# Performance work log

Hardware: AMD Instinct MI355X
Metric: run time of the kernel (lower is better)

The kernel has to match this reference:

```python
import jax, jax.numpy as jnp
import numpy as np

D_MODEL = 256
N_HEADS = 4
WINDOW = 8
DECAY = 0.9
STEP_SIZE = 0.5


def _linear(x, w, b):
    # torch nn.Linear: y = x @ w.T + b, w: [out, in]
    return jnp.einsum('...i,oi->...o', x, w) + b


def _layernorm(x, scale, bias, eps=1e-5):
    mu = jnp.mean(x, axis=-1, keepdims=True)
    var = jnp.var(x, axis=-1, keepdims=True)
    return (x - mu) * jax.lax.rsqrt(var + eps) * scale + bias


def _ema(x, decay):
    # ema[t] = decay*ema[t-1] + (1-decay)*x[t], ema[-1]=0
    # (exactly the causal conv with weights (1-d)*d^i from the torch code)
    def step(c, xt):
        c = decay * c + (1.0 - decay) * xt
        return c, c
    _, ys = jax.lax.scan(step, jnp.zeros_like(x[:, 0]), jnp.swapaxes(x, 0, 1))
    return jnp.swapaxes(ys, 0, 1)


def setup_inputs() -> dict:
    key = jax.random.key(0)
    ks = iter(jax.random.split(key, 40))
    B, T, D = 8, 1024, D_MODEL
    s = 0.02
    inp = {
        'parallel_repr': jax.random.normal(next(ks), (B, T, D), jnp.float32),
        'sequential_state': jax.random.normal(next(ks), (B, D), jnp.float32),
        'trajectory_summary': jax.random.normal(next(ks), (B, D), jnp.float32),
        # MultiheadAttention params
        'in_proj_w': jax.random.normal(next(ks), (3 * D, D), jnp.float32) * s,
        'in_proj_b': jnp.zeros((3 * D,), jnp.float32),
        'out_proj_w': jax.random.normal(next(ks), (D, D), jnp.float32) * s,
        'out_proj_b': jnp.zeros((D,), jnp.float32),
        # depthwise causal conv (local history)
        'conv_w': jax.random.normal(next(ks), (D, 1, WINDOW), jnp.float32) * s,
        'conv_b': jnp.zeros((D,), jnp.float32),
        # parallel_to_sequential / sequential_to_parallel
        'p2s_w': jax.random.normal(next(ks), (D, D), jnp.float32) * s,
        'p2s_b': jnp.zeros((D,), jnp.float32),
        's2p_w': jax.random.normal(next(ks), (D, D), jnp.float32) * s,
        's2p_b': jnp.zeros((D,), jnp.float32),
        # transition MLP: 3D -> 2D -> D
        'trans_w1': jax.random.normal(next(ks), (2 * D, 3 * D), jnp.float32) * s,
        'trans_b1': jnp.zeros((2 * D,), jnp.float32),
        'trans_w2': jax.random.normal(next(ks), (D, 2 * D), jnp.float32) * s,
        'trans_b2': jnp.zeros((D,), jnp.float32),
        # FFN: D -> 4D -> D
        'ffn_w1': jax.random.normal(next(ks), (4 * D, D), jnp.float32) * s,
        'ffn_b1': jnp.zeros((4 * D,), jnp.float32),
        'ffn_w2': jax.random.normal(next(ks), (D, 4 * D), jnp.float32) * s,
        'ffn_b2': jnp.zeros((D,), jnp.float32),
        # LayerNorms
        'ln1_s': jnp.ones((D,), jnp.float32), 'ln1_b': jnp.zeros((D,), jnp.float32),
        'ln2_s': jnp.ones((D,), jnp.float32), 'ln2_b': jnp.zeros((D,), jnp.float32),
        'ln3_s': jnp.ones((D,), jnp.float32), 'ln3_b': jnp.zeros((D,), jnp.float32),
        'ln4_s': jnp.ones((D,), jnp.float32), 'ln4_b': jnp.zeros((D,), jnp.float32),
    }
    return inp


def _forward(parallel_repr, sequential_state,
             in_proj_w, in_proj_b, out_proj_w, out_proj_b,
             conv_w, conv_b, p2s_w, p2s_b, s2p_w, s2p_b,
             trans_w1, trans_b1, trans_w2, trans_b2,
             ffn_w1, ffn_b1, ffn_w2, ffn_b2,
             ln1_s, ln1_b, ln2_s, ln2_b, ln3_s, ln3_b, ln4_s, ln4_b):
    B, T, D = parallel_repr.shape
    H, hd = N_HEADS, D // N_HEADS

    # --- causal self-attention (nn.MultiheadAttention, batch_first) ---
    qkv = _linear(parallel_repr, in_proj_w, in_proj_b)
    q, k, v = jnp.split(qkv, 3, axis=-1)
    q = q.reshape(B, T, H, hd)
    k = k.reshape(B, T, H, hd)
    v = v.reshape(B, T, H, hd)
    scores = jnp.einsum('bqhd,bkhd->bhqk', q, k) / jnp.sqrt(jnp.asarray(hd, q.dtype))
    causal = jnp.triu(jnp.ones((T, T), bool), 1)
    scores = jnp.where(causal, jnp.finfo(scores.dtype).min, scores)
    attn = jax.nn.softmax(scores, axis=-1)
    attn_out = jnp.einsum('bhqk,bkhd->bqhd', attn, v).reshape(B, T, D)
    attn_out = _linear(attn_out, out_proj_w, out_proj_b)
    x = _layernorm(parallel_repr + attn_out, ln1_s, ln1_b)

    # --- depthwise causal conv (local history) ---
    xt = jnp.swapaxes(x, 1, 2)  # [B, D, T]
    xt_pad = jnp.pad(xt, ((0, 0), (0, 0), (WINDOW - 1, 0)))
    local = jax.lax.conv_general_dilated(
        xt_pad, conv_w, window_strides=(1,), padding='VALID',
        dimension_numbers=('NCH', 'OIH', 'NCH'), feature_group_count=D)
    local_history = jnp.swapaxes(local + conv_b[None, :, None], 1, 2)  # [B, T, D]

    # --- global EMA summary ---
    global_summary = _ema(x, DECAY)

    # --- transition deltas + cumsum state integration ---
    parallel_guidance = _linear(x, p2s_w, p2s_b)
    combined = jnp.concatenate([x + 0.3 * parallel_guidance, local_history, global_summary], axis=-1)
    h = jax.nn.gelu(_linear(combined, trans_w1, trans_b1), approximate=False)
    deltas = _linear(h, trans_w2, trans_b2)
    states = sequential_state[:, None, :] + jnp.cumsum(deltas, axis=1) * STEP_SIZE
    states = _layernorm(states, ln3_s, ln3_b)

    # --- FFN with sequential guidance ---
    seq_guidance = _linear(states, s2p_w, s2p_b)
    f = jax.nn.gelu(_linear(x + 0.3 * seq_guidance, ffn_w1, ffn_b1), approximate=False)
    ffn_out = _linear(f, ffn_w2, ffn_b2)
    x = _layernorm(x + ffn_out, ln2_s, ln2_b)

    final_sequential_state = _layernorm(states[:, -1, :], ln4_s, ln4_b)
    final_trajectory_summary = global_summary[:, -1, :]
    return x, final_sequential_state, final_trajectory_summary


def reference(parallel_repr, sequential_state, trajectory_summary,
              in_proj_w, in_proj_b, out_proj_w, out_proj_b,
              conv_w, conv_b, p2s_w, p2s_b, s2p_w, s2p_b,
              trans_w1, trans_b1, trans_w2, trans_b2,
              ffn_w1, ffn_b1, ffn_w2, ffn_b2,
              ln1_s, ln1_b, ln2_s, ln2_b, ln3_s, ln3_b, ln4_s, ln4_b):
    # trajectory_summary is accepted by the torch forward but never used.
    return _forward(parallel_repr, sequential_state,
                    in_proj_w, in_proj_b, out_proj_w, out_proj_b,
                    conv_w, conv_b, p2s_w, p2s_b, s2p_w, s2p_b,
                    trans_w1, trans_b1, trans_w2, trans_b2,
                    ffn_w1, ffn_b1, ffn_w2, ffn_b2,
                    ln1_s, ln1_b, ln2_s, ln2_b, ln3_s, ln3_b, ln4_s, ln4_b)
```

## Files before the change

kernel.cpp:

```cpp
#include <hip/hip_runtime.h>
#include <math.h>

typedef unsigned short u16;
typedef __attribute__((ext_vector_type(8))) short bf16x8;
typedef __attribute__((ext_vector_type(4))) float f32x4;

#define D_MODEL 256
#define T_SZ 1024
constexpr size_t S_ELT = (size_t)8192 * 256;
constexpr size_t MB = 1024 * 1024;

constexpr size_t OFF_QKV = 0;
constexpr size_t OFF_ATTN = 12 * MB;
constexpr size_t OFF_F = 0;
constexpr size_t OFF_X = 16 * MB;
constexpr size_t OFF_COMB = 24 * MB;
constexpr size_t OFF_FB = 36 * MB;
constexpr size_t OFF_H = 44 * MB;
constexpr size_t OFF_WB = 52 * MB;
constexpr int WB_INPROJ = 0;
constexpr int WB_OUTPROJ = 196608;
constexpr int WB_P2S = 262144;
constexpr int WB_S2P = 327680;
constexpr int WB_T1 = 393216;
constexpr int WB_T2 = 786432;
constexpr int WB_F1 = 917504;
constexpr int WB_F2 = 1179648;
constexpr int WB_TOTAL = 1441792;
constexpr int PR_TOTAL = 2097152;
constexpr size_t OFF_B1E = OFF_WB + (size_t)WB_TOTAL * 2;
constexpr size_t OFF_B1E2 = OFF_B1E + 4096;
constexpr size_t OFF_WC2 = 55 * MB;
constexpr size_t OFF_SCR1 = 55 * MB + 524288;
constexpr size_t OFF_SCR2 = 55 * MB + 786432;

__device__ __forceinline__ u16 f2bf(float f) {
  unsigned int u = __float_as_uint(f);
  u += 0x7fff + ((u >> 16) & 1);
  return (u16)(u >> 16);
}
__device__ __forceinline__ float bf2f(u16 s) {
  return __uint_as_float(((unsigned int)s) << 16);
}

__device__ __forceinline__ void glds16(const u16* g, u16* l) {
  __builtin_amdgcn_global_load_lds(
      (const __attribute__((address_space(1))) void*)g,
      (__attribute__((address_space(3))) void*)l, 16, 0, 0);
}

__global__ __launch_bounds__(256)
void wconv_kernel(const float* w0, const float* w1, const float* w2,
                  const float* w3, const float* w4, const float* w5,
                  const float* w6, const float* w7, const float* pr,
                  u16* __restrict__ wb, u16* __restrict__ prb) {
  const int idx4 = (blockIdx.x * 256 + threadIdx.x) * 4;
  if (idx4 < WB_TOTAL) {
    const int offs[9] = {WB_INPROJ, WB_OUTPROJ, WB_P2S,  WB_S2P, WB_T1,
                         WB_T2,     WB_F1,      WB_F2,   WB_TOTAL};
    const float* srcs[8] = {w0, w1, w2, w3, w4, w5, w6, w7};
    int seg = 0;
    while (idx4 >= offs[seg + 1]) ++seg;
    float4 v = *(const float4*)(srcs[seg] + (idx4 - offs[seg]));
    unsigned int lo = (unsigned int)f2bf(v.x) | ((unsigned int)f2bf(v.y) << 16);
    unsigned int hi = (unsigned int)f2bf(v.z) | ((unsigned int)f2bf(v.w) << 16);
    *(uint2*)(wb + idx4) = make_uint2(lo, hi);
  } else {
    const int i4 = idx4 - WB_TOTAL;
    if (i4 < PR_TOTAL) {
      float4 v = *(const float4*)(pr + i4);
      unsigned int lo = (unsigned int)f2bf(v.x) | ((unsigned int)f2bf(v.y) << 16);
      unsigned int hi = (unsigned int)f2bf(v.z) | ((unsigned int)f2bf(v.w) << 16);
      *(uint2*)(prb + i4) = make_uint2(lo, hi);
    }
  }
}

__global__ __launch_bounds__(256)
void wfold_kernel(const float* __restrict__ t1, const float* __restrict__ p2s,
                  const float* __restrict__ t1b, const float* __restrict__ p2sb,
                  const float* __restrict__ f1, const float* __restrict__ s2p,
                  const float* __restrict__ f1b, const float* __restrict__ s2pb,
                  u16* __restrict__ wt1, float* __restrict__ b1e,
                  u16* __restrict__ wc2, float* __restrict__ b1e2) {
  __shared__ float trow[8][256];
  const int blk = blockIdx.x;
  const int k = threadIdx.x;
  const bool t1role = blk < 64;
  const int o0 = t1role ? blk * 8 : (blk - 64) * 8;
  const float* wsrc = t1role ? t1 : f1;
  const int wstride = t1role ? 768 : 256;
  const float* psrc = t1role ? p2s : s2p;
  const float* pbsrc = t1role ? p2sb : s2pb;
#pragma unroll
  for (int r = 0; r < 8; ++r)
    trow[r][k] = wsrc[(size_t)(o0 + r) * wstride + k];
  __syncthreads();
  float acc[8] = {};
  float bacc[8] = {};
  for (int i = 0; i < 256; ++i) {
    const float pv = psrc[(size_t)i * 256 + k];
    const float pbv = pbsrc[i];
#pragma unroll
    for (int r = 0; r < 8; ++r) {
      acc[r] = fmaf(trow[r][i], pv, acc[r]);
      bacc[r] = fmaf(trow[r][i], pbv, bacc[r]);
    }
  }
  if (t1role) {
#pragma unroll
    for (int r = 0; r < 8; ++r)
      wt1[(size_t)(o0 + r) * 768 + k] = f2bf(trow[r][k] + 0.3f * acc[r]);
    if (k == 0) {
#pragma unroll
      for (int r = 0; r < 8; ++r)
        b1e[o0 + r] = t1b[o0 + r] + 0.3f * bacc[r];
    }
  } else {
#pragma unroll
    for (int r = 0; r < 8; ++r)
      wc2[(size_t)(o0 + r) * 256 + k] = f2bf(0.3f * acc[r]);
    if (k == 0) {
#pragma unroll
      for (int r = 0; r < 8; ++r)
        b1e2[o0 + r] = f1b[o0 + r] + 0.3f * bacc[r];
    }
  }
}

enum { EPI_NONE = 0, EPI_GELU = 1 };

template <int EPI, int BM, int BN, bool OUTBF, bool VSPLIT, bool SPLIT>
__global__ __launch_bounds__(256, 4)
void mgemm(const u16* __restrict__ A, int lda, const u16* __restrict__ A2,
           const u16* __restrict__ Wb, int ldb, const u16* __restrict__ B2,
           int K, const float* __restrict__ bias, void* __restrict__ Cv,
           int ldc, int col_off, u16* __restrict__ vt) {
  __shared__ u16 As[2 * BM * 64];
  __shared__ u16 Bs[2 * BN * 64];
  const int tid = threadIdx.x;
  const int w = tid >> 6, lane = tid & 63;
  const int ln = lane & 15, quad = lane >> 4;
  const int m0 = blockIdx.x * BM;
  const int n0 = blockIdx.y * BN;
  constexpr int MT = (BM == 128) ? 2 : 1;
  const int wm = w * (MT * 16);
  constexpr int APW = BM / 64;
  constexpr int BPW = BN / 64;

  f32x4 acc[MT][4] = {};

  const int grow = lane >> 2;
  const int gk8 = (lane & 3) * 8;

#define STAGE_MM(k0s, buf)                                                    \
  {                                                                           \
    const u16* Ag; const u16* Bg; int as_, bs_, kk;                           \
    if (!SPLIT || (k0s) < 256) {                                              \
      Ag = A; as_ = lda; Bg = Wb; bs_ = ldb; kk = (k0s);                      \
    } else {                                                                  \
      Ag = A2; as_ = 256; Bg = B2; bs_ = 256; kk = (k0s)-256;                 \
    }                                                                         \
    _Pragma("unroll") for (int s = 0; s < 2; ++s) {                           \
      _Pragma("unroll") for (int p = 0; p < APW; ++p) {                       \
        const int g = w * APW + p;                                            \
        glds16(Ag + (size_t)(m0 + g * 16 + grow) * as_ + kk + s * 32 + gk8,   \
               As + (buf) * (BM * 64) + s * BM * 32 + g * 512);               \
      }                                                                       \
      _Pragma("unroll") for (int p = 0; p < BPW; ++p) {                       \
        const int g = w * BPW + p;                                            \
        glds16(Bg + (size_t)(n0 + g * 16 + grow) * bs_ + kk + s * 32 + gk8,   \
               Bs + (buf) * (BN * 64) + s * BN * 32 + g * 512);               \
      }                                                                       \
    }                                                                         \
  }

  int cur = 0;
  STAGE_MM(0, 0);
  for (int k0 = 0; k0 < K; k0 += 64) {
    __syncthreads();
    if (k0 + 64 < K) STAGE_MM(k0 + 64, cur ^ 1);
#pragma unroll
    for (int s = 0; s < 2; ++s) {
      const u16* abase =
          As + cur * (BM * 64) + s * BM * 32 + (wm >> 4) * 512 + ln * 32 + quad * 8;
      const u16* bbase = Bs + cur * (BN * 64) + s * BN * 32 + ln * 32 + quad * 8;
      bf16x8 af[MT], bv[4];
#pragma unroll
      for (int i = 0; i < MT; ++i) af[i] = *(const bf16x8*)(abase + i * 512);
#pragma unroll
      for (int j = 0; j < 4; ++j) bv[j] = *(const bf16x8*)(bbase + j * 512);
#pragma unroll
      for (int i = 0; i < MT; ++i)
#pragma unroll
        for (int j = 0; j < 4; ++j)
          acc[i][j] = __builtin_amdgcn_mfma_f32_16x16x32_bf16(af[i], bv[j],
                                                              acc[i][j], 0, 0, 0);
    }
    cur ^= 1;
  }
#undef STAGE_MM

#pragma unroll
  for (int i = 0; i < MT; ++i)
#pragma unroll
    for (int j = 0; j < 4; ++j) {
      const int col = n0 + j * 16 + ln;
      const float bsv = bias[col];
      const int row0 = m0 + wm + i * 16 + quad * 4;
      float vals[4];
#pragma unroll
      for (int r = 0; r < 4; ++r) {
        float v = acc[i][j][r] + bsv;
        if (EPI == EPI_GELU) v = 0.5f * v * (1.0f + erff(v * 0.70710678f));
        vals[r] = v;
      }
      if (VSPLIT && col >= 512) {
        ushort4 pk;
        pk.x = f2bf(vals[0]); pk.y = f2bf(vals[1]);
        pk.z = f2bf(vals[2]); pk.w = f2bf(vals[3]);
        *(ushort4*)(vt + (size_t)((row0 >> 10) * 256 + (col - 512)) * T_SZ +
                    (row0 & 1023)) = pk;
      } else if (OUTBF) {
#pragma unroll
        for (int r = 0; r < 4; ++r)
          ((u16*)Cv)[(size_t)(row0 + r) * ldc + col_off + col] = f2bf(vals[r]);
      } else {
#pragma unroll
        for (int r = 0; r < 4; ++r)
          ((float*)Cv)[(size_t)(row0 + r) * ldc + col_off + col] = vals[r];
      }
    }
}

template <bool WRITE_BF>
__global__ __launch_bounds__(256, 4)
void mgemm_ln16(const u16* __restrict__ A, const u16* __restrict__ Wb, int K,
                const float* __restrict__ bias, const float* __restrict__ addsrc,
                const float* __restrict__ g, const float* __restrict__ bb,
                float* __restrict__ outf, u16* __restrict__ outbf, int bfldc) {
  __shared__ u16 As[2 * 1024];
  __shared__ u16 Bs[2 * 16384];
  __shared__ float tS1[4][16], tS2[4][16];
  const int tid = threadIdx.x;
  const int w = tid >> 6, lane = tid & 63;
  const int ln = lane & 15, quad = lane >> 4;
  const int m0 = blockIdx.x * 16;
  const int grow = lane >> 2;
  const int gk8 = (lane & 3) * 8;

  f32x4 acc[4] = {};

#define STAGE_LN(k0s, buf)                                                    \
  {                                                                           \
    if (w < 2)                                                                \
      glds16(A + (size_t)(m0 + grow) * K + (k0s) + w * 32 + gk8,              \
             As + (buf) * 1024 + w * 512);                                    \
    _Pragma("unroll") for (int p = 0; p < 8; ++p) {                           \
      const int idx = w * 8 + p;                                              \
      const int s = idx >> 4, gg = idx & 15;                                  \
      glds16(Wb + (size_t)(gg * 16 + grow) * K + (k0s) + s * 32 + gk8,        \
             Bs + (buf) * 16384 + s * 8192 + gg * 512);                       \
    }                                                                         \
  }

  int cur = 0;
  STAGE_LN(0, 0);
  for (int k0 = 0; k0 < K; k0 += 64) {
    __syncthreads();
    if (k0 + 64 < K) STAGE_LN(k0 + 64, cur ^ 1);
#pragma unroll
    for (int s = 0; s < 2; ++s) {
      const bf16x8 af =
          *(const bf16x8*)(As + cur * 1024 + s * 512 + ln * 32 + quad * 8);
      const u16* bbase =
          Bs + cur * 16384 + s * 8192 + (w * 4) * 512 + ln * 32 + quad * 8;
#pragma unroll
      for (int j = 0; j < 4; ++j) {
        bf16x8 bv = *(const bf16x8*)(bbase + j * 512);
        acc[j] = __builtin_amdgcn_mfma_f32_16x16x32_bf16(af, bv, acc[j], 0, 0, 0);
      }
    }
    cur ^= 1;
  }
#undef STAGE_LN

  const int row0 = m0 + quad * 4;
  float s1[4] = {}, s2[4] = {};
#pragma unroll
  for (int j = 0; j < 4; ++j) {
    const int col = w * 64 + j * 16 + ln;
    const float bsv = bias[col];
#pragma unroll
    for (int r = 0; r < 4; ++r) {
      float v = acc[j][r] + bsv + addsrc[(size_t)(row0 + r) * 256 + col];
      acc[j][r] = v;
      s1[r] += v;
      s2[r] += v * v;
    }
  }
#pragma unroll
  for (int r = 0; r < 4; ++r) {
#pragma unroll
    for (int o = 8; o > 0; o >>= 1) {
      s1[r] += __shfl_xor(s1[r], o);
      s2[r] += __shfl_xor(s2[r], o);
    }
  }
  __syncthreads();
  if (ln == 0) {
#pragma unroll
    for (int r = 0; r < 4; ++r) {
      tS1[w][quad * 4 + r] = s1[r];
      tS2[w][quad * 4 + r] = s2[r];
    }
  }
  __syncthreads();
  float mean[4], inv[4];
#pragma unroll
  for (int r = 0; r < 4; ++r) {
    const int qr = quad * 4 + r;
    const float S1 = tS1[0][qr] + tS1[1][qr] + tS1[2][qr] + tS1[3][qr];
    const float S2 = tS2[0][qr] + tS2[1][qr] + tS2[2][qr] + tS2[3][qr];
    mean[r] = S1 * (1.f / 256.f);
    const float var = S2 * (1.f / 256.f) - mean[r] * mean[r];
    inv[r] = rsqrtf(var + 1e-5f);
  }
#pragma unroll
  for (int j = 0; j < 4; ++j) {
    const int col = w * 64 + j * 16 + ln;
    const float gc = g[col], bc = bb[col];
#pragma unroll
    for (int r = 0; r < 4; ++r) {
      const float y = (acc[j][r] - mean[r]) * inv[r] * gc + bc;
      outf[(size_t)(row0 + r) * 256 + col] = y;
      if (WRITE_BF) outbf[(size_t)(row0 + r) * bfldc + col] = f2bf(y);
    }
  }
}

__global__ __launch_bounds__(256)
void attn_flash(const u16* __restrict__ qkv, const u16* __restrict__ vt,
                u16* __restrict__ outp) {
  __shared__ u16 Ks[2][4096];
  __shared__ u16 Vs[2][4096];
  __shared__ u16 Ps[4][16][72];
  const int tid = threadIdx.x;
  const int w = tid >> 6, lane = tid & 63;
  const int ln = lane & 15, quad = lane >> 4, kq8 = quad * 8;
  const int bid = blockIdx.x;
  const int r0 = bid & 255;
  int bh = r0 >> 4;
  int p = r0 & 15;
  if (bid >> 8) { bh += 16; p = 15 - p; }
  const int qt = p * 4 + w;
  const int q0 = qt * 16;
  const int b = bh >> 2, h = bh & 3;
  const u16* base = qkv + (size_t)b * T_SZ * 768;
  const u16* kbase = base + 256 + h * 64;
  const u16* vbase = vt + (size_t)bh * 64 * T_SZ;
  const int grow = lane >> 2;
  const int gk8 = (lane & 3) * 8;

  bf16x8 qf[2];
#pragma unroll
  for (int ks = 0; ks < 2; ++ks)
    qf[ks] = *(const bf16x8*)(base + (size_t)(q0 + ln) * 768 + h * 64 +
                              ks * 32 + kq8);
  const short ob = (short)0x3F80;
  const bf16x8 ones = {ob, ob, ob, ob, ob, ob, ob, ob};

  const int nt = p + 1;

#define STAGE_KV(jt, buf)                                                     \
  {                                                                           \
    const int c0s = (jt) * 64;                                                \
    const int isV = w >> 1, ss = w & 1;                                       \
    _Pragma("unroll") for (int pg = 0; pg < 4; ++pg) {                        \
      if (!isV)                                                               \
        glds16(kbase + (size_t)(c0s + pg * 16 + grow) * 768 + ss * 32 + gk8,  \
               &Ks[buf][ss * 2048 + pg * 512]);                               \
      else                                                                    \
        glds16(vbase + (size_t)(pg * 16 + grow) * T_SZ + c0s + ss * 32 + gk8, \
               &Vs[buf][ss * 2048 + pg * 512]);                               \
    }                                                                         \
  }

  f32x4 O[4] = {};
  f32x4 l_acc = {};
  int cur = 0;
  STAGE_KV(0, 0);
  for (int jt = 0; jt < nt; ++jt) {
    __syncthreads();
    if (jt + 1 < nt) STAGE_KV(jt + 1, cur ^ 1);
    const int c0 = jt * 64;
    f32x4 sv[4] = {};
#pragma unroll
    for (int ks = 0; ks < 2; ++ks)
#pragma unroll
      for (int j = 0; j < 4; ++j) {
        bf16x8 kf = *(const bf16x8*)&Ks[cur][ks * 2048 + j * 512 + ln * 32 + kq8];
        sv[j] = __builtin_amdgcn_mfma_f32_16x16x32_bf16(qf[ks], kf, sv[j], 0, 0, 0);
      }
    const bool need_mask = (jt == nt - 1);
#pragma unroll
    for (int j = 0; j < 4; ++j)
#pragma unroll
      for (int r = 0; r < 4; ++r) {
        float pv = __expf(sv[j][r] * 0.125f);
        if (need_mask && (c0 + j * 16 + ln > q0 + quad * 4 + r)) pv = 0.f;
        Ps[w][quad * 4 + r][j * 16 + ln] = f2bf(pv);
      }
#pragma unroll
    for (int ks = 0; ks < 2; ++ks) {
      bf16x8 pf = *(const bf16x8*)&Ps[w][ln][ks * 32 + kq8];
      l_acc = __builtin_amdgcn_mfma_f32_16x16x32_bf16(pf, ones, l_acc, 0, 0, 0);
#pragma unroll
      for (int j = 0; j < 4; ++j) {
        bf16x8 vf = *(const bf16x8*)&Vs[cur][ks * 2048 + j * 512 + ln * 32 + kq8];
        O[j] = __builtin_amdgcn_mfma_f32_16x16x32_bf16(pf, vf, O[j], 0, 0, 0);
      }
    }
    cur ^= 1;
  }
#undef STAGE_KV

  u16* op = outp + (size_t)b * T_SZ * 256;
#pragma unroll
  for (int r = 0; r < 4; ++r) {
    const float inv = 1.f / l_acc[r];
#pragma unroll
    for (int j = 0; j < 4; ++j)
      op[(size_t)(q0 + quad * 4 + r) * 256 + h * 64 + j * 16 + ln] =
          f2bf(O[j][r] * inv);
  }
}

__device__ __forceinline__ void block_reduce_2(float& a, float& q, float* tmp) {
#pragma unroll
  for (int o = 32; o > 0; o >>= 1) {
    a += __shfl_down(a, o);
    q += __shfl_down(q, o);
  }
  const int lane = threadIdx.x & 63, wid = threadIdx.x >> 6;
  if (lane == 0) { tmp[wid] = a; tmp[4 + wid] = q; }
  __syncthreads();
  a = tmp[0] + tmp[1] + tmp[2] + tmp[3];
  q = tmp[4] + tmp[5] + tmp[6] + tmp[7];
  __syncthreads();
}

__device__ __forceinline__ float ln_finish(float v, float s1, float s2,
                                           float g, float bb) {
  float mean = s1 * (1.f / 256.f);
  float var = s2 * (1.f / 256.f) - mean * mean;
  return (v - mean) * rsqrtf(var + 1e-5f) * g + bb;
}

__global__ __launch_bounds__(256)
void emaconv_kernel(const float* __restrict__ x, const float* __restrict__ cw,
                    const float* __restrict__ cb, u16* __restrict__ comb,
                    float* __restrict__ scr) {
  const int bc = blockIdx.x;
  const int b = bc >> 5, ch = bc & 31;
  const int d = threadIdx.x;
  const int t0 = ch * 32;
  float wreg[8];
#pragma unroll
  for (int j = 0; j < 8; ++j) wreg[j] = cw[d * 8 + j];
  const float bias = cb[d];
  float xw[8];
#pragma unroll
  for (int j = 0; j < 7; ++j) {
    const int ts = t0 - 7 + j;
    xw[j] = (ts >= 0) ? x[(size_t)(b * T_SZ + ts) * 256 + d] : 0.f;
  }
  float c = 0.f;
#pragma unroll
  for (int tl = 0; tl < 32; ++tl) {
    const size_t row = (size_t)(b * T_SZ + t0 + tl);
    xw[7] = x[row * 256 + d];
    float conv = bias;
#pragma unroll
    for (int j = 0; j < 8; ++j) conv = fmaf(xw[j], wreg[j], conv);
    c = 0.9f * c + 0.1f * xw[7];
    comb[row * 768 + 256 + d] = f2bf(conv);
    comb[row * 768 + 512 + d] = f2bf(c);
#pragma unroll
    for (int j = 0; j < 7; ++j) xw[j] = xw[j + 1];
  }
  scr[(size_t)bc * 256 + d] = c;
}

__global__ __launch_bounds__(256)
void ema_b_kernel(float* __restrict__ scr) {
  const int b = blockIdx.x, d = threadIdx.x;
  const float q32 = 0.03433683820292512f;
  float carry = 0.f;
  for (int ch = 0; ch < 32; ++ch) {
    const size_t idx = (size_t)(b * 32 + ch) * 256 + d;
    float e = scr[idx];
    scr[idx] = carry;
    carry = e + q32 * carry;
  }
}

__global__ __launch_bounds__(256)
void ema_c_kernel(u16* __restrict__ comb, const float* __restrict__ scr,
                  float* __restrict__ fts) {
  const int row = blockIdx.x;
  const int b = row >> 10, t = row & 1023;
  const int d = threadIdx.x;
  const int ch = t >> 5, tl = t & 31;
  float carry = scr[(size_t)(b * 32 + ch) * 256 + d];
  float l = bf2f(comb[(size_t)row * 768 + 512 + d]);
  float y = fmaf(__powf(0.9f, (float)(tl + 1)), carry, l);
  comb[(size_t)row * 768 + 512 + d] = f2bf(y);
  if (t == 1023) fts[b * 256 + d] = y;
}

__global__ __launch_bounds__(256)
void cs_a_kernel(float* __restrict__ deltas, float* __restrict__ scr) {
  const int bc = blockIdx.x;
  const int b = bc >> 5, ch = bc & 31;
  const int d = threadIdx.x;
  const int t0 = ch * 32;
  float c = 0.f;
  for (int tl = 0; tl < 32; ++tl) {
    const size_t idx = (size_t)(b * T_SZ + t0 + tl) * 256 + d;
    c += deltas[idx];
    deltas[idx] = c;
  }
  scr[(size_t)bc * 256 + d] = c;
}

__global__ __launch_bounds__(256)
void cs_b_kernel(float* __restrict__ scr) {
  const int b = blockIdx.x, d = threadIdx.x;
  float carry = 0.f;
  for (int ch = 0; ch < 32; ++ch) {
    const size_t idx = (size_t)(b * 32 + ch) * 256 + d;
    float e = scr[idx];
    scr[idx] = carry;
    carry += e;
  }
}

__global__ __launch_bounds__(256)
void ln3_states_kernel(const float* __restrict__ deltas, const float* __restrict__ scr,
                       const float* __restrict__ seq, const float* __restrict__ g3,
                       const float* __restrict__ b3, const float* __restrict__ g4,
                       const float* __restrict__ b4, u16* __restrict__ st,
                       float* __restrict__ fss) {
  __shared__ float tmp[8];
  const int row = blockIdx.x;
  const int b = row >> 10, t = row & 1023;
  const int d = threadIdx.x;
  float v = seq[b * 256 + d] +
            0.5f * (deltas[(size_t)row * 256 + d] +
                    scr[(size_t)(b * 32 + (t >> 5)) * 256 + d]);
  float a = v, q = v * v;
  block_reduce_2(a, q, tmp);
  const float y = ln_finish(v, a, q, g3[d], b3[d]);
  st[(size_t)row * 256 + d] = f2bf(y);
  if (t == 1023) {
    float a2 = y, q2 = y * y;
    block_reduce_2(a2, q2, tmp);
    fss[b * 256 + d] = ln_finish(y, a2, q2, g4[d], b4[d]);
  }
}

extern "C" void kernel_launch(void* const* d_in, const int* in_sizes, int n_in,
                              void* d_out, int out_size, void* d_ws,
                              size_t ws_size, hipStream_t stream) {
  (void)in_sizes; (void)n_in; (void)out_size; (void)ws_size;
  const float* parallel_repr = (const float*)d_in[0];
  const float* sequential_state = (const float*)d_in[1];
  const float* in_proj_b = (const float*)d_in[4];
  const float* out_proj_b = (const float*)d_in[6];
  const float* conv_w = (const float*)d_in[7];
  const float* conv_b = (const float*)d_in[8];
  const float* p2s_w_f = (const float*)d_in[9];
  const float* p2s_b = (const float*)d_in[10];
  const float* s2p_w_f = (const float*)d_in[11];
  const float* s2p_b = (const float*)d_in[12];
  const float* trans_w1_f = (const float*)d_in[13];
  const float* trans_b1 = (const float*)d_in[14];
  const float* trans_b2 = (const float*)d_in[16];
  const float* ffn_w1_f = (const float*)d_in[17];
  const float* ffn_b1 = (const float*)d_in[18];
  const float* ffn_b2 = (const float*)d_in[20];
  const float* ln1_s = (const float*)d_in[21];
  const float* ln1_b = (const float*)d_in[22];
  const float* ln2_s = (const float*)d_in[23];
  const float* ln2_b = (const float*)d_in[24];
  const float* ln3_s = (const float*)d_in[25];
  const float* ln3_b = (const float*)d_in[26];
  const float* ln4_s = (const float*)d_in[27];
  const float* ln4_b = (const float*)d_in[28];

  char* ws = (char*)d_ws;
  u16* qkv_bf = (u16*)(ws + OFF_QKV);
  u16* attn_bf = (u16*)(ws + OFF_ATTN);
  u16* states_bf = (u16*)(ws + OFF_ATTN);
  u16* f_bf = (u16*)(ws + OFF_F);
  float* x = (float*)(ws + OFF_X);
  u16* comb = (u16*)(ws + OFF_COMB);
  u16* pr_bf = (u16*)(ws + OFF_COMB);
  float* fbuf = (float*)(ws + OFF_FB);
  u16* vt = (u16*)(ws + OFF_H);
  u16* h_bf = (u16*)(ws + OFF_H);
  u16* wb = (u16*)(ws + OFF_WB);
  u16* wc2 = (u16*)(ws + OFF_WC2);
  float* scr1 = (float*)(ws + OFF_SCR1);
  float* scr2 = (float*)(ws + OFF_SCR2);
  float* b1e = (float*)(ws + OFF_B1E);
  float* b1e2 = (float*)(ws + OFF_B1E2);
  float* out = (float*)d_out;
  float* out_fss = out + S_ELT;
  float* out_fts = out + S_ELT + 2048;

  const dim3 blk(256);

  wconv_kernel<<<3456, blk, 0, stream>>>(
      (const float*)d_in[3], (const float*)d_in[5], (const float*)d_in[9],
      (const float*)d_in[11], (const float*)d_in[13], (const float*)d_in[15],
      (const float*)d_in[17], (const float*)d_in[19], parallel_repr, wb, pr_bf);
  wfold_kernel<<<192, blk, 0, stream>>>(trans_w1_f, p2s_w_f, trans_b1, p2s_b,
                                        ffn_w1_f, s2p_w_f, ffn_b1, s2p_b,
                                        wb + WB_T1, b1e, wc2, b1e2);
  mgemm<EPI_NONE, 128, 64, true, true, false><<<dim3(64, 12), blk, 0, stream>>>(
      pr_bf, 256, nullptr, wb + WB_INPROJ, 256, nullptr, 256, in_proj_b,
      qkv_bf, 768, 0, vt);
  attn_flash<<<512, blk, 0, stream>>>(qkv_bf, vt, attn_bf);
  mgemm_ln16<true><<<512, blk, 0, stream>>>(
      attn_bf, wb + WB_OUTPROJ, 256, out_proj_b, parallel_repr, ln1_s, ln1_b,
      x, comb, 768);
  emaconv_kernel<<<256, blk, 0, stream>>>(x, conv_w, conv_b, comb, scr1);
  ema_b_kernel<<<8, blk, 0, stream>>>(scr1);
  ema_c_kernel<<<8192, blk, 0, stream>>>(comb, scr1, out_fts);
  mgemm<EPI_GELU, 128, 64, true, false, false><<<dim3(64, 8), blk, 0, stream>>>(
      comb, 768, nullptr, wb + WB_T1, 768, nullptr, 768, b1e, h_bf, 512, 0,
      nullptr);
  mgemm<EPI_NONE, 64, 64, false, false, false><<<dim3(128, 4), blk, 0, stream>>>(
      h_bf, 512, nullptr, wb + WB_T2, 512, nullptr, 512, trans_b2, fbuf, 256,
      0, nullptr);
  cs_a_kernel<<<256, blk, 0, stream>>>(fbuf, scr2);
  cs_b_kernel<<<8, blk, 0, stream>>>(scr2);
  ln3_states_kernel<<<8192, blk, 0, stream>>>(fbuf, scr2, sequential_state,
                                              ln3_s, ln3_b, ln4_s, ln4_b,
                                              states_bf, out_fss);
  mgemm<EPI_GELU, 128, 64, true, false, true><<<dim3(64, 16), blk, 0, stream>>>(
      comb, 768, states_bf, wb + WB_F1, 256, wc2, 512, b1e2, f_bf, 1024, 0,
      nullptr);
  mgemm_ln16<false><<<512, blk, 0, stream>>>(
      f_bf, wb + WB_F2, 1024, ffn_b2, x, ln2_s, ln2_b, out, nullptr, 256);
}
```

Baseline: 263.3 us.

## Merge weight prep kernels, fuse chunked cumsum into GEMM epilogue, vectorize EMA fixup

After: 269.7 us. +2.4%, slower.

```diff
diff --git a/kernel.cpp b/kernel.cpp
--- a/kernel.cpp
+++ b/kernel.cpp
@@ -50,92 +50,96 @@
 }
 
 __global__ __launch_bounds__(256)
-void wconv_kernel(const float* w0, const float* w1, const float* w2,
+void wprep_kernel(const float* w0, const float* w1, const float* w2,
                   const float* w3, const float* w4, const float* w5,
                   const float* w6, const float* w7, const float* pr,
-                  u16* __restrict__ wb, u16* __restrict__ prb) {
-  const int idx4 = (blockIdx.x * 256 + threadIdx.x) * 4;
-  if (idx4 < WB_TOTAL) {
-    const int offs[9] = {WB_INPROJ, WB_OUTPROJ, WB_P2S,  WB_S2P, WB_T1,
-                         WB_T2,     WB_F1,      WB_F2,   WB_TOTAL};
-    const float* srcs[8] = {w0, w1, w2, w3, w4, w5, w6, w7};
-    int seg = 0;
-    while (idx4 >= offs[seg + 1]) ++seg;
-    float4 v = *(const float4*)(srcs[seg] + (idx4 - offs[seg]));
-    unsigned int lo = (unsigned int)f2bf(v.x) | ((unsigned int)f2bf(v.y) << 16);
-    unsigned int hi = (unsigned int)f2bf(v.z) | ((unsigned int)f2bf(v.w) << 16);
-    *(uint2*)(wb + idx4) = make_uint2(lo, hi);
+                  u16* __restrict__ wb, u16* __restrict__ prb,
+                  const float* __restrict__ t1b, const float* __restrict__ p2sb,
+                  const float* __restrict__ f1b, const float* __restrict__ s2pb,
+                  float* __restrict__ b1e, u16* __restrict__ wc2,
+                  float* __restrict__ b1e2) {
+  __shared__ float trow[8][256];
+  const int bx = blockIdx.x;
+  if (bx < 3456) {
+    const int idx4 = (bx * 256 + threadIdx.x) * 4;
+    if (idx4 < WB_TOTAL) {
+      const int offs[9] = {WB_INPROJ, WB_OUTPROJ, WB_P2S,  WB_S2P, WB_T1,
+                           WB_T2,     WB_F1,      WB_F2,   WB_TOTAL};
+      const float* srcs[8] = {w0, w1, w2, w3, w4, w5, w6, w7};
+      int seg = 0;
+      while (idx4 >= offs[seg + 1]) ++seg;
+      const bool skip = (seg == 4) && (((idx4 - WB_T1) % 768) < 256);
+      if (!skip) {
+        float4 v = *(const float4*)(srcs[seg] + (idx4 - offs[seg]));
+        unsigned int lo = (unsigned int)f2bf(v.x) | ((unsigned int)f2bf(v.y) << 16);
+        unsigned int hi = (unsigned int)f2bf(v.z) | ((unsigned int)f2bf(v.w) << 16);
+        *(uint2*)(wb + idx4) = make_uint2(lo, hi);
+      }
+    } else {
+      const int i4 = idx4 - WB_TOTAL;
+      if (i4 < PR_TOTAL) {
+        float4 v = *(const float4*)(pr + i4);
+        unsigned int lo = (unsigned int)f2bf(v.x) | ((unsigned int)f2bf(v.y) << 16);
+        unsigned int hi = (unsigned int)f2bf(v.z) | ((unsigned int)f2bf(v.w) << 16);
+        *(uint2*)(prb + i4) = make_uint2(lo, hi);
+      }
+    }
   } else {
-    const int i4 = idx4 - WB_TOTAL;
-    if (i4 < PR_TOTAL) {
-      float4 v = *(const float4*)(pr + i4);
-      unsigned int lo = (unsigned int)f2bf(v.x) | ((unsigned int)f2bf(v.y) << 16);
-      unsigned int hi = (unsigned int)f2bf(v.z) | ((unsigned int)f2bf(v.w) << 16);
-      *(uint2*)(prb + i4) = make_uint2(lo, hi);
-    }
-  }
-}
-
-__global__ __launch_bounds__(256)
-void wfold_kernel(const float* __restrict__ t1, const float* __restrict__ p2s,
-                  const float* __restrict__ t1b, const float* __restrict__ p2sb,
-                  const float* __restrict__ f1, const float* __restrict__ s2p,
-                  const float* __restrict__ f1b, const float* __restrict__ s2pb,
-                  u16* __restrict__ wt1, float* __restrict__ b1e,
-                  u16* __restrict__ wc2, float* __restrict__ b1e2) {
-  __shared__ float trow[8][256];
-  const int blk = blockIdx.x;
-  const int k = threadIdx.x;
-  const bool t1role = blk < 64;
-  const int o0 = t1role ? blk * 8 : (blk - 64) * 8;
-  const float* wsrc = t1role ? t1 : f1;
-  const int wstride = t1role ? 768 : 256;
-  const float* psrc = t1role ? p2s : s2p;
-  const float* pbsrc = t1role ? p2sb : s2pb;
-#pragma unroll
-  for (int r = 0; r < 8; ++r)
-    trow[r][k] = wsrc[(size_t)(o0 + r) * wstride + k];
-  __syncthreads();
-  float acc[8] = {};
-  float bacc[8] = {};
-  for (int i = 0; i < 256; ++i) {
-    const float pv = psrc[(size_t)i * 256 + k];
-    const float pbv = pbsrc[i];
-#pragma unroll
-    for (int r = 0; r < 8; ++r) {
-      acc[r] = fmaf(trow[r][i], pv, acc[r]);
-      bacc[r] = fmaf(trow[r][i], pbv, bacc[r]);
-    }
-  }
-  if (t1role) {
+    const int blk = bx - 3456;
+    const int k = threadIdx.x;
+    const bool t1role = blk < 64;
+    const int o0 = t1role ? blk * 8 : (blk - 64) * 8;
+    const float* wsrc = t1role ? w4 : w6;
+    const int wstride = t1role ? 768 : 256;
+    const float* psrc = t1role ? w2 : w3;
+    const float* pbsrc = t1role ? p2sb : s2pb;
 #pragma unroll
     for (int r = 0; r < 8; ++r)
-      wt1[(size_t)(o0 + r) * 768 + k] = f2bf(trow[r][k] + 0.3f * acc[r]);
-    if (k == 0) {
+      trow[r][k] = wsrc[(size_t)(o0 + r) * wstride + k];
+    __syncthreads();
+    float acc[8] = {};
+    float bacc[8] = {};
+    for (int i = 0; i < 256; ++i) {
+      const float pv = psrc[(size_t)i * 256 + k];
+      const float pbv = pbsrc[i];
+#pragma unroll
+      for (int r = 0; r < 8; ++r) {
+        acc[r] = fmaf(trow[r][i], pv, acc[r]);
+        bacc[r] = fmaf(trow[r][i], pbv, bacc[r]);
+      }
+    }
+    if (t1role) {
+      u16* wt1 = wb + WB_T1;
 #pragma unroll
       for (int r = 0; r < 8; ++r)
-        b1e[o0 + r] = t1b[o0 + r] + 0.3f * bacc[r];
-    }
-  } else {
-#pragma unroll
-    for (int r = 0; r < 8; ++r)
-      wc2[(size_t)(o0 + r) * 256 + k] = f2bf(0.3f * acc[r]);
-    if (k == 0) {
+        wt1[(size_t)(o0 + r) * 768 + k] = f2bf(trow[r][k] + 0.3f * acc[r]);
+      if (k == 0) {
+#pragma unroll
+        for (int r = 0; r < 8; ++r)
+          b1e[o0 + r] = t1b[o0 + r] + 0.3f * bacc[r];
+      }
+    } else {
 #pragma unroll
       for (int r = 0; r < 8; ++r)
-        b1e2[o0 + r] = f1b[o0 + r] + 0.3f * bacc[r];
+        wc2[(size_t)(o0 + r) * 256 + k] = f2bf(0.3f * acc[r]);
+      if (k == 0) {
+#pragma unroll
+        for (int r = 0; r < 8; ++r)
+          b1e2[o0 + r] = f1b[o0 + r] + 0.3f * bacc[r];
+      }
     }
   }
 }
 
 enum { EPI_NONE = 0, EPI_GELU = 1 };
 
-template <int EPI, int BM, int BN, bool OUTBF, bool VSPLIT, bool SPLIT>
+template <int EPI, int BM, int BN, bool OUTBF, bool VSPLIT, bool SPLIT, bool CSUM>
 __global__ __launch_bounds__(256, 4)
 void mgemm(const u16* __restrict__ A, int lda, const u16* __restrict__ A2,
            const u16* __restrict__ Wb, int ldb, const u16* __restrict__ B2,
            int K, const float* __restrict__ bias, void* __restrict__ Cv,
-           int ldc, int col_off, u16* __restrict__ vt) {
+           int ldc, int col_off, u16* __restrict__ vt,
+           float* __restrict__ csum) {
   __shared__ u16 As[2 * BM * 64];
   __shared__ u16 Bs[2 * BN * 64];
   const int tid = threadIdx.x;
@@ -200,6 +204,45 @@
     cur ^= 1;
   }
 #undef STAGE_MM
+
+  if constexpr (CSUM) {
+    __shared__ float halfsum[4][64];
+    const int row0 = m0 + wm + quad * 4;
+    float lp[4][4], qex[4];
+#pragma unroll
+    for (int j = 0; j < 4; ++j) {
+      const float bsv = bias[n0 + j * 16 + ln];
+      float run = 0.f;
+#pragma unroll
+      for (int r = 0; r < 4; ++r) {
+        run += acc[0][j][r] + bsv;
+        lp[j][r] = run;
+      }
+      float sq = run;
+      float u = __shfl_up(sq, 16);
+      if (quad >= 1) sq += u;
+      u = __shfl_up(sq, 32);
+      if (quad >= 2) sq += u;
+      qex[j] = sq - run;
+      if (quad == 3) halfsum[w][j * 16 + ln] = sq;
+    }
+    __syncthreads();
+#pragma unroll
+    for (int j = 0; j < 4; ++j) {
+      const float base = (w & 1) ? halfsum[w - 1][j * 16 + ln] : 0.f;
+#pragma unroll
+      for (int r = 0; r < 4; ++r)
+        ((float*)Cv)[(size_t)(row0 + r) * ldc + n0 + j * 16 + ln] =
+            lp[j][r] + qex[j] + base;
+    }
+    if (tid < 128) {
+      const int c = tid & 63, chi = tid >> 6;
+      const int bb_ = m0 >> 10, ch0 = (m0 & 1023) >> 5;
+      csum[(size_t)(bb_ * 32 + ch0 + chi) * 256 + n0 + c] =
+          halfsum[2 * chi][c] + halfsum[2 * chi + 1][c];
+    }
+    return;
+  }
 
 #pragma unroll
   for (int i = 0; i < MT; ++i)
@@ -508,30 +551,26 @@
 __global__ __launch_bounds__(256)
 void ema_c_kernel(u16* __restrict__ comb, const float* __restrict__ scr,
                   float* __restrict__ fts) {
-  const int row = blockIdx.x;
+  const int row = blockIdx.x * 4 + (threadIdx.x >> 6);
+  const int d4 = (threadIdx.x & 63) * 4;
   const int b = row >> 10, t = row & 1023;
-  const int d = threadIdx.x;
   const int ch = t >> 5, tl = t & 31;
-  float carry = scr[(size_t)(b * 32 + ch) * 256 + d];
-  float l = bf2f(comb[(size_t)row * 768 + 512 + d]);
-  float y = fmaf(__powf(0.9f, (float)(tl + 1)), carry, l);
-  comb[(size_t)row * 768 + 512 + d] = f2bf(y);
-  if (t == 1023) fts[b * 256 + d] = y;
-}
-
-__global__ __launch_bounds__(256)
-void cs_a_kernel(float* __restrict__ deltas, float* __restrict__ scr) {
-  const int bc = blockIdx.x;
-  const int b = bc >> 5, ch = bc & 31;
-  const int d = threadIdx.x;
-  const int t0 = ch * 32;
-  float c = 0.f;
-  for (int tl = 0; tl < 32; ++tl) {
-    const size_t idx = (size_t)(b * T_SZ + t0 + tl) * 256 + d;
-    c += deltas[idx];
-    deltas[idx] = c;
-  }
-  scr[(size_t)bc * 256 + d] = c;
+  const float4 cv = *(const float4*)(scr + (size_t)(b * 32 + ch) * 256 + d4);
+  const float pw = __powf(0.9f, (float)(tl + 1));
+  u16* cp = comb + (size_t)row * 768 + 512 + d4;
+  ushort4 lv = *(ushort4*)cp;
+  float y0 = fmaf(pw, cv.x, bf2f(lv.x));
+  float y1 = fmaf(pw, cv.y, bf2f(lv.y));
+  float y2 = fmaf(pw, cv.z, bf2f(lv.z));
+  float y3 = fmaf(pw, cv.w, bf2f(lv.w));
+  ushort4 ov;
+  ov.x = f2bf(y0); ov.y = f2bf(y1); ov.z = f2bf(y2); ov.w = f2bf(y3);
+  *(ushort4*)cp = ov;
+  if (t == 1023) {
+    float4 fo;
+    fo.x = y0; fo.y = y1; fo.z = y2; fo.w = y3;
+    *(float4*)(fts + b * 256 + d4) = fo;
+  }
 }
 
 __global__ __launch_bounds__(256)
@@ -580,14 +619,10 @@
   const float* out_proj_b = (const float*)d_in[6];
   const float* conv_w = (const float*)d_in[7];
   const float* conv_b = (const float*)d_in[8];
-  const float* p2s_w_f = (const float*)d_in[9];
   const float* p2s_b = (const float*)d_in[10];
-  const float* s2p_w_f = (const float*)d_in[11];
   const float* s2p_b = (const float*)d_in[12];
-  const float* trans_w1_f = (const float*)d_in[13];
   const float* trans_b1 = (const float*)d_in[14];
   const float* trans_b2 = (const float*)d_in[16];
-  const float* ffn_w1_f = (const float*)d_in[17];
   const float* ffn_b1 = (const float*)d_in[18];
   const float* ffn_b2 = (const float*)d_in[20];
   const float* ln1_s = (const float*)d_in[21];
@@ -622,37 +657,38 @@
 
   const dim3 blk(256);
 
-  wconv_kernel<<<3456, blk, 0, stream>>>(
+  wprep_kernel<<<3648, blk, 0, stream>>>(
       (const float*)d_in[3], (const float*)d_in[5], (const float*)d_in[9],
       (const float*)d_in[11], (const float*)d_in[13], (const float*)d_in[15],
-      (const float*)d_in[17], (const float*)d_in[19], parallel_repr, wb, pr_bf);
-  wfold_kernel<<<192, blk, 0, stream>>>(trans_w1_f, p2s_w_f, trans_b1, p2s_b,
-                                        ffn_w1_f, s2p_w_f, ffn_b1, s2p_b,
-                                        wb + WB_T1, b1e, wc2, b1e2);
-  mgemm<EPI_NONE, 128, 64, true, true, false><<<dim3(64, 12), blk, 0, stream>>>(
-      pr_bf, 256, nullptr, wb + WB_INPROJ, 256, nullptr, 256, in_proj_b,
-      qkv_bf, 768, 0, vt);
+      (const float*)d_in[17], (const float*)d_in[19], parallel_repr, wb, pr_bf,
+      trans_b1, p2s_b, ffn_b1, s2p_b, b1e, wc2, b1e2);
+  mgemm<EPI_NONE, 128, 64, true, true, false, false>
+      <<<dim3(64, 12), blk, 0, stream>>>(pr_bf, 256, nullptr, wb + WB_INPROJ,
+                                         256, nullptr, 256, in_proj_b, qkv_bf,
+                                         768, 0, vt, nullptr);
   attn_flash<<<512, blk, 0, stream>>>(qkv_bf, vt, attn_bf);
   mgemm_ln16<true><<<512, blk, 0, stream>>>(
       attn_bf, wb + WB_OUTPROJ, 256, out_proj_b, parallel_repr, ln1_s, ln1_b,
       x, comb, 768);
   emaconv_kernel<<<256, blk, 0, stream>>>(x, conv_w, conv_b, comb, scr1);
   ema_b_kernel<<<8, blk, 0, stream>>>(scr1);
-  ema_c_kernel<<<8192, blk, 0, stream>>>(comb, scr1, out_fts);
-  mgemm<EPI_GELU, 128, 64, true, false, false><<<dim3(64, 8), blk, 0, stream>>>(
-      comb, 768, nullptr, wb + WB_T1, 768, nullptr, 768, b1e, h_bf, 512, 0,
-      nullptr);
-  mgemm<EPI_NONE, 64, 64, false, false, false><<<dim3(128, 4), blk, 0, stream>>>(
-      h_bf, 512, nullptr, wb + WB_T2, 512, nullptr, 512, trans_b2, fbuf, 256,
-      0, nullptr);
-  cs_a_kernel<<<256, blk, 0, stream>>>(fbuf, scr2);
+  ema_c_kernel<<<2048, blk, 0, stream>>>(comb, scr1, out_fts);
+  mgemm<EPI_GELU, 128, 64, true, false, false, false>
+      <<<dim3(64, 8), blk, 0, stream>>>(comb, 768, nullptr, wb + WB_T1, 768,
+                                        nullptr, 768, b1e, h_bf, 512, 0,
+                                        nullptr, nullptr);
+  mgemm<EPI_NONE, 64, 64, false, false, false, true>
+      <<<dim3(128, 4), blk, 0, stream>>>(h_bf, 512, nullptr, wb + WB_T2, 512,
+                                         nullptr, 512, trans_b2, fbuf, 256, 0,
+                                         nullptr, scr2);
   cs_b_kernel<<<8, blk, 0, stream>>>(scr2);
   ln3_states_kernel<<<8192, blk, 0, stream>>>(fbuf, scr2, sequential_state,
                                               ln3_s, ln3_b, ln4_s, ln4_b,
                                               states_bf, out_fss);
-  mgemm<EPI_GELU, 128, 64, true, false, true><<<dim3(64, 16), blk, 0, stream>>>(
-      comb, 768, states_bf, wb + WB_F1, 256, wc2, 512, b1e2, f_bf, 1024, 0,
-      nullptr);
+  mgemm<EPI_GELU, 128, 64, true, false, true, false>
+      <<<dim3(64, 16), blk, 0, stream>>>(comb, 768, states_bf, wb + WB_F1, 256,
+                                         wc2, 512, b1e2, f_bf, 1024, 0,
+                                         nullptr, nullptr);
   mgemm_ln16<false><<<512, blk, 0, stream>>>(
       f_bf, wb + WB_F2, 1024, ffn_b2, x, ln2_s, ln2_b, out, nullptr, 256);
 }
```
